# Optimization experiments

Hardware: AMD Instinct MI355X
Metric: run time of the kernel (lower is better)

## Reference

```python
import jax, jax.numpy as jnp
import numpy as np
from jax import lax

B, L, P, CIN, N, HD, PH, K = 2048, 96, 96, 8, 64, 64, 8, 3
DIM_C = CIN * N  # 512


def _silu(x):
    return x * jax.nn.sigmoid(x)


def _lin(x, w, b):
    return x @ w.T + b


def setup_inputs() -> dict:
    key = jax.random.key(0)
    ks = iter(jax.random.split(key, 64))

    def w(shape):
        fan_in = shape[-1]
        return (jax.random.normal(next(ks), shape, jnp.float32) / np.sqrt(fan_in)).astype(jnp.float32)

    inp = {"x": jax.random.normal(next(ks), (B, L, CIN), jnp.float32)}
    # x_proj: 5 Linears (enc_in->h, h->h, h->h, h->h, h->N), SiLU between (dropout=eval/identity)
    inp["xp_w0"] = w((HD, CIN)); inp["xp_b0"] = jnp.zeros((HD,), jnp.float32)
    inp["xp_w1"] = w((HD, HD));  inp["xp_b1"] = jnp.zeros((HD,), jnp.float32)
    inp["xp_w2"] = w((HD, HD));  inp["xp_b2"] = jnp.zeros((HD,), jnp.float32)
    inp["xp_w3"] = w((HD, HD));  inp["xp_b3"] = jnp.zeros((HD,), jnp.float32)
    inp["xp_w4"] = w((N, HD));   inp["xp_b4"] = jnp.zeros((N,), jnp.float32)
    # x_proj_: Linear(N,h), SiLU, Linear(h,N)
    inp["xpp_w0"] = w((HD, N)); inp["xpp_b0"] = jnp.zeros((HD,), jnp.float32)
    inp["xpp_w1"] = w((N, HD)); inp["xpp_b1"] = jnp.zeros((N,), jnp.float32)
    # depthwise dilated Conv1d: weight (N, 1, K)
    inp["conv_w"] = w((N, 1, K)); inp["conv_b"] = jnp.zeros((N,), jnp.float32)
    inp["span_A"] = jnp.asarray(0.1, jnp.float32)
    # compress: Linear(N*L, PH)
    inp["comp_w"] = w((PH, N * L)); inp["comp_b"] = jnp.zeros((PH,), jnp.float32)
    # a_ode.net: Linear(PH,h), SiLU, Linear(h,PH), Tanh
    inp["net_w0"] = w((HD, PH)); inp["net_b0"] = jnp.zeros((HD,), jnp.float32)
    inp["net_w1"] = w((PH, HD)); inp["net_b1"] = jnp.zeros((PH,), jnp.float32)
    # lat2out: Linear(PH,8), SiLU, Linear(8,N)
    inp["lo_w0"] = w((8, PH)); inp["lo_b0"] = jnp.zeros((8,), jnp.float32)
    inp["lo_w1"] = w((N, 8));  inp["lo_b1"] = jnp.zeros((N,), jnp.float32)
    # lat2out_c: Linear(PH,8), SiLU, Linear(8, CIN*N)
    inp["lc_w0"] = w((8, PH));     inp["lc_b0"] = jnp.zeros((8,), jnp.float32)
    inp["lc_w1"] = w((DIM_C, 8));  inp["lc_b1"] = jnp.zeros((DIM_C,), jnp.float32)
    # lat2out_z: Linear(N,N), SiLU, Linear(N, CIN)
    inp["lz_w0"] = w((N, N));   inp["lz_b0"] = jnp.zeros((N,), jnp.float32)
    inp["lz_w1"] = w((CIN, N)); inp["lz_b1"] = jnp.zeros((CIN,), jnp.float32)
    return inp


def reference(x, xp_w0, xp_b0, xp_w1, xp_b1, xp_w2, xp_b2, xp_w3, xp_b3, xp_w4, xp_b4,
              xpp_w0, xpp_b0, xpp_w1, xpp_b1, conv_w, conv_b, span_A, comp_w, comp_b,
              net_w0, net_b0, net_w1, net_b1, lo_w0, lo_b0, lo_w1, lo_b1,
              lc_w0, lc_b0, lc_w1, lc_b1, lz_w0, lz_b0, lz_w1, lz_b1):
    Bsz = x.shape[0]

    def x_proj(t):
        h = _silu(_lin(t, xp_w0, xp_b0))
        h = _silu(_lin(h, xp_w1, xp_b1))
        h = _silu(_lin(h, xp_w2, xp_b2))
        h = _silu(_lin(h, xp_w3, xp_b3))
        return _lin(h, xp_w4, xp_b4)

    x_old = x_proj(x[:, :L])                       # (B, L, N)
    hist = x_old.transpose(0, 2, 1)                # (B, N, L)
    pad = (K - 1) * 2                              # 4
    conv = lax.conv_general_dilated(
        hist, conv_w, window_strides=(1,), padding=[(pad, pad)],
        rhs_dilation=(2,), dimension_numbers=("NCH", "OIH", "NCH"),
        feature_group_count=N) + conv_b[None, :, None]
    hist = _silu(conv)[:, :, -L:]                  # (B, N, L)
    hist_f = hist.transpose(0, 2, 1).reshape(Bsz, L * N)
    vector_F = _lin(hist_f, comp_w, comp_b)        # (B, PH)

    a0 = vector_F
    z0 = x_proj(x[:, L - 1])                       # (B, N)

    # Householder matrix H = I - 2 v v^T with v = normalize(x_proj_(z0))
    v = _lin(_silu(_lin(z0, xpp_w0, xpp_b0)), xpp_w1, xpp_b1)
    v = v / (jnp.linalg.norm(v, axis=-1, keepdims=True) + 1e-8)
    Hh = jnp.eye(N, dtype=x.dtype)[None] - 2.0 * v[:, :, None] * v[:, None, :]  # (B,N,N)

    dt = jnp.clip(span_A, 1e-8, 7.0)               # uniform Euler step size
    s0 = jnp.concatenate([a0, z0], axis=-1)        # (B, PH+N)

    def step(s, _):
        a = s[:, :PH]
        z = s[:, PH:]
        da = jnp.tanh(_lin(_silu(_lin(a, net_w0, net_b0)), net_w1, net_b1))  # (B,PH)
        d = _lin(_silu(_lin(a, lo_w0, lo_b0)), lo_w1, lo_b1)                 # (B,N)
        # dz = H^T diag(d) H z   (fused; avoids materializing A_mat)
        Hz = jnp.einsum('bjk,bk->bj', Hh, z)
        dz = jnp.einsum('bj,bji->bi', d * Hz, Hh)
        s_new = s + dt * jnp.concatenate([da, dz], axis=-1)
        return s_new, s_new

    _, sol = lax.scan(step, s0, None, length=P)    # (P, B, PH+N) == sol[1:]

    c_traj = sol[:, :, :PH]                        # (P, B, PH)
    z_traj = sol[:, :, PH:]                        # (P, B, N)

    C = _lin(_silu(_lin(c_traj, lc_w0, lc_b0)), lc_w1, lc_b1)  # (P, B, CIN*N)
    C = C.reshape(P, Bsz, CIN, N)
    y_hat_c = jnp.einsum('pbcn,pbn->pbc', C, z_traj)           # (P, B, CIN)
    added_z = _lin(_silu(_lin(z_traj, lz_w0, lz_b0)), lz_w1, lz_b1)
    x_pred = (y_hat_c + added_z).transpose(1, 0, 2)            # (B, P, CIN)

    x_rec = x[:, :L, :]
    return (x_rec, x_pred)
```

## Files before the change

### kernel.cpp

```cpp
#include <hip/hip_runtime.h>
#include <cstdint>
#include <cstddef>

#define BB 2048
#define LL 96
#define PP 96
#define NN 64
#define HSTRIDE 68

typedef __attribute__((ext_vector_type(8))) short short8;
typedef __attribute__((ext_vector_type(4))) float f32x4;

union U4S8 { uint4 u; short8 s; };

__device__ __forceinline__ float siluf(float x) {
  return x * __builtin_amdgcn_rcpf(1.0f + __expf(-x));
}
__device__ __forceinline__ float tanhf_fast(float x) {
  return 1.0f - 2.0f * __builtin_amdgcn_rcpf(1.0f + __expf(2.0f * x));
}
__device__ __forceinline__ float rlane(float x, int l) {
  return __int_as_float(__builtin_amdgcn_readlane(__float_as_int(x), l));
}

template <int CTRL>
__device__ __forceinline__ float dppadd(float x) {
  int y = __builtin_amdgcn_update_dpp(0, __float_as_int(x), CTRL, 0xF, 0xF, false);
  return x + __int_as_float(y);
}
template <int CTRL>
__device__ __forceinline__ float dppmov(float x) {
  int y = __builtin_amdgcn_update_dpp(0, __float_as_int(x), CTRL, 0xF, 0xF, false);
  return __int_as_float(y);
}

__device__ __forceinline__ float addswap16(float x) {
#if __has_builtin(__builtin_amdgcn_permlane16_swap)
  auto r = __builtin_amdgcn_permlane16_swap(__float_as_uint(x), __float_as_uint(x), false, false);
  return __uint_as_float(r[0]) + __uint_as_float(r[1]);
#else
  return x + __shfl_xor(x, 16, 64);
#endif
}
__device__ __forceinline__ float addswap32(float x) {
#if __has_builtin(__builtin_amdgcn_permlane32_swap)
  auto r = __builtin_amdgcn_permlane32_swap(__float_as_uint(x), __float_as_uint(x), false, false);
  return __uint_as_float(r[0]) + __uint_as_float(r[1]);
#else
  return x + __shfl_xor(x, 32, 64);
#endif
}
__device__ __forceinline__ float movswap32(float x, bool hi) {
#if __has_builtin(__builtin_amdgcn_permlane32_swap)
  auto r = __builtin_amdgcn_permlane32_swap(__float_as_uint(x), __float_as_uint(x), false, false);
  return __uint_as_float(hi ? r[0] : r[1]);
#else
  return __shfl_xor(x, 32, 64);
#endif
}

__device__ __forceinline__ float wave_sum(float x) {
  x = dppadd<0xB1>(x);
  x = dppadd<0x4E>(x);
  x = dppadd<0x141>(x);
  x = dppadd<0x128>(x);
  x = addswap16(x);
  x = addswap32(x);
  return x;
}

__device__ __forceinline__ uint32_t packsplit(float f) {
  uint32_t b = __float_as_uint(f);
  uint32_t h = b & 0xFFFF0000u;
  float r = f - __uint_as_float(h);
  return h | (__float_as_uint(r) >> 16);
}
__device__ __forceinline__ void splitpack2(float f0, float f1, uint32_t& dhi, uint32_t& dlo) {
  uint32_t b0 = __float_as_uint(f0), b1 = __float_as_uint(f1);
  uint32_t h0 = b0 & 0xFFFF0000u, h1 = b1 & 0xFFFF0000u;
  float r0 = f0 - __uint_as_float(h0), r1 = f1 - __uint_as_float(h1);
  dhi = (h0 >> 16) | h1;
  dlo = (__float_as_uint(r0) >> 16) | (__float_as_uint(r1) & 0xFFFF0000u);
}
__device__ __forceinline__ void unpack2(uint32_t p0, uint32_t p1, uint32_t& dhi, uint32_t& dlo) {
  dhi = (p0 >> 16) | (p1 & 0xFFFF0000u);
  dlo = (p0 & 0xFFFFu) | (p1 << 16);
}
__device__ __forceinline__ void readfrag(const uint32_t* p, short8& hi, short8& lo) {
  uint4 pa = *(const uint4*)p;
  uint4 pb = *(const uint4*)(p + 4);
  U4S8 h, l;
  unpack2(pa.x, pa.y, h.u.x, l.u.x);
  unpack2(pa.z, pa.w, h.u.y, l.u.y);
  unpack2(pb.x, pb.y, h.u.z, l.u.z);
  unpack2(pb.z, pb.w, h.u.w, l.u.w);
  hi = h.s; lo = l.s;
}
__device__ __forceinline__ f32x4 mm_split(f32x4 acc, const short8* Ah, const short8* Al,
                                          const short8* Bh, const short8* Bl) {
  acc = __builtin_amdgcn_mfma_f32_16x16x32_bf16(Ah[0], Bh[0], acc, 0, 0, 0);
  acc = __builtin_amdgcn_mfma_f32_16x16x32_bf16(Ah[1], Bh[1], acc, 0, 0, 0);
  acc = __builtin_amdgcn_mfma_f32_16x16x32_bf16(Al[0], Bh[0], acc, 0, 0, 0);
  acc = __builtin_amdgcn_mfma_f32_16x16x32_bf16(Al[1], Bh[1], acc, 0, 0, 0);
  acc = __builtin_amdgcn_mfma_f32_16x16x32_bf16(Ah[0], Bl[0], acc, 0, 0, 0);
  acc = __builtin_amdgcn_mfma_f32_16x16x32_bf16(Ah[1], Bl[1], acc, 0, 0, 0);
  return acc;
}

__global__ __launch_bounds__(256, 2) void k_xproj(
    const float* __restrict__ x,
    const float* __restrict__ w0, const float* __restrict__ b0,
    const float* __restrict__ w1, const float* __restrict__ b1,
    const float* __restrict__ w2, const float* __restrict__ b2,
    const float* __restrict__ w3, const float* __restrict__ b3,
    const float* __restrict__ w4, const float* __restrict__ b4,
    float* __restrict__ x_old, float* __restrict__ out)
{
  __shared__ uint32_t hbuf[128 * HSTRIDE];
  __shared__ uint32_t wbufA[64 * HSTRIDE];
  __shared__ uint32_t wbufB[64 * HSTRIDE];
  __shared__ float bs[320];

  int tid = threadIdx.x;
  int wave = tid >> 6, lane = tid & 63;
  int quad = lane >> 4, m16 = lane & 15;
  size_t tokBase = (size_t)blockIdx.x * 128;

  {
    size_t e = tokBase * 8 + (size_t)tid * 4;
    *(float4*)(out + e) = *(const float4*)(x + e);
  }
  if (tid < 64) {
    bs[tid]       = b0[tid];
    bs[64 + tid]  = b1[tid];
    bs[128 + tid] = b2[tid];
    bs[192 + tid] = b3[tid];
    bs[256 + tid] = b4[tid];
  }
  #pragma unroll
  for (int i = 0; i < 4; ++i) {
    int e4 = i * 256 + tid;
    int o = e4 >> 4, k = (e4 & 15) << 2;
    float4 wv = ((const float4*)w1)[e4];
    *(uint4*)(wbufA + o * HSTRIDE + k) =
        make_uint4(packsplit(wv.x), packsplit(wv.y), packsplit(wv.z), packsplit(wv.w));
  }
  __syncthreads();

  short8 A0h[2], A0l[2];
  #pragma unroll
  for (int mt = 0; mt < 2; ++mt) {
    U4S8 h, l;
    h.u = make_uint4(0, 0, 0, 0); l.u = make_uint4(0, 0, 0, 0);
    if (quad == 0) {
      const float* xp = x + (tokBase + wave * 32 + mt * 16 + m16) * 8;
      float4 xa = *(const float4*)xp;
      float4 xb = *(const float4*)(xp + 4);
      splitpack2(xa.x, xa.y, h.u.x, l.u.x);
      splitpack2(xa.z, xa.w, h.u.y, l.u.y);
      splitpack2(xb.x, xb.y, h.u.z, l.u.z);
      splitpack2(xb.z, xb.w, h.u.w, l.u.w);
    }
    A0h[mt] = h.s; A0l[mt] = l.s;
  }
  short8 B0h[4], B0l[4];
  #pragma unroll
  for (int nt = 0; nt < 4; ++nt) {
    U4S8 h, l;
    h.u = make_uint4(0, 0, 0, 0); l.u = make_uint4(0, 0, 0, 0);
    if (quad == 0) {
      const float* wp = w0 + (nt * 16 + m16) * 8;
      float4 wa = *(const float4*)wp;
      float4 wb = *(const float4*)(wp + 4);
      splitpack2(wa.x, wa.y, h.u.x, l.u.x);
      splitpack2(wa.z, wa.w, h.u.y, l.u.y);
      splitpack2(wb.x, wb.y, h.u.z, l.u.z);
      splitpack2(wb.z, wb.w, h.u.w, l.u.w);
    }
    B0h[nt] = h.s; B0l[nt] = l.s;
  }
  {
    f32x4 acc[2][4];
    #pragma unroll
    for (int mt = 0; mt < 2; ++mt)
      #pragma unroll
      for (int nt = 0; nt < 4; ++nt) {
        float bv = bs[nt * 16 + m16];
        acc[mt][nt] = (f32x4){bv, bv, bv, bv};
      }
    #pragma unroll
    for (int mt = 0; mt < 2; ++mt)
      #pragma unroll
      for (int nt = 0; nt < 4; ++nt)
        acc[mt][nt] = __builtin_amdgcn_mfma_f32_16x16x32_bf16(A0h[mt], B0h[nt], acc[mt][nt], 0, 0, 0);
    #pragma unroll
    for (int mt = 0; mt < 2; ++mt)
      #pragma unroll
      for (int nt = 0; nt < 4; ++nt)
        acc[mt][nt] = __builtin_amdgcn_mfma_f32_16x16x32_bf16(A0l[mt], B0h[nt], acc[mt][nt], 0, 0, 0);
    #pragma unroll
    for (int mt = 0; mt < 2; ++mt)
      #pragma unroll
      for (int nt = 0; nt < 4; ++nt)
        acc[mt][nt] = __builtin_amdgcn_mfma_f32_16x16x32_bf16(A0h[mt], B0l[nt], acc[mt][nt], 0, 0, 0);
    #pragma unroll
    for (int mt = 0; mt < 2; ++mt)
      #pragma unroll
      for (int nt = 0; nt < 4; ++nt)
        #pragma unroll
        for (int r = 0; r < 4; ++r) {
          float s = siluf(acc[mt][nt][r]);
          hbuf[(wave * 32 + mt * 16 + quad * 4 + r) * HSTRIDE + nt * 16 + m16] = packsplit(s);
        }
  }

  const float* Ws[4] = {w1, w2, w3, w4};
  uint32_t* cur = wbufA;
  uint32_t* nxt = wbufB;
  #pragma unroll 1
  for (int lyr = 0; lyr < 4; ++lyr) {
    float4 wv[4];
    if (lyr < 3) {
      const float* wn = Ws[lyr + 1];
      #pragma unroll
      for (int i = 0; i < 4; ++i) wv[i] = ((const float4*)wn)[i * 256 + tid];
    }
    short8 Bh[8], Bl[8];
    #pragma unroll
    for (int nt = 0; nt < 4; ++nt)
      #pragma unroll
      for (int ks = 0; ks < 2; ++ks)
        readfrag(cur + (nt * 16 + m16) * HSTRIDE + ks * 32 + quad * 8, Bh[nt * 2 + ks], Bl[nt * 2 + ks]);
    short8 Ah[4], Al[4];
    #pragma unroll
    for (int mt = 0; mt < 2; ++mt)
      #pragma unroll
      for (int ks = 0; ks < 2; ++ks)
        readfrag(hbuf + (wave * 32 + mt * 16 + m16) * HSTRIDE + ks * 32 + quad * 8, Ah[mt * 2 + ks], Al[mt * 2 + ks]);

    f32x4 acc[2][4];
    #pragma unroll
    for (int mt = 0; mt < 2; ++mt)
      #pragma unroll
      for (int nt = 0; nt < 4; ++nt) {
        float bv = bs[(lyr + 1) * 64 + nt * 16 + m16];
        acc[mt][nt] = (f32x4){bv, bv, bv, bv};
      }
    #pragma unroll
    for (int ks = 0; ks < 2; ++ks)
      #pragma unroll
      for (int mt = 0; mt < 2; ++mt)
        #pragma unroll
        for (int nt = 0; nt < 4; ++nt)
          acc[mt][nt] = __builtin_amdgcn_mfma_f32_16x16x32_bf16(Ah[mt * 2 + ks], Bh[nt * 2 + ks], acc[mt][nt], 0, 0, 0);
    #pragma unroll
    for (int ks = 0; ks < 2; ++ks)
      #pragma unroll
      for (int mt = 0; mt < 2; ++mt)
        #pragma unroll
        for (int nt = 0; nt < 4; ++nt)
          acc[mt][nt] = __builtin_amdgcn_mfma_f32_16x16x32_bf16(Al[mt * 2 + ks], Bh[nt * 2 + ks], acc[mt][nt], 0, 0, 0);
    #pragma unroll
    for (int ks = 0; ks < 2; ++ks)
      #pragma unroll
      for (int mt = 0; mt < 2; ++mt)
        #pragma unroll
        for (int nt = 0; nt < 4; ++nt)
          acc[mt][nt] = __builtin_amdgcn_mfma_f32_16x16x32_bf16(Ah[mt * 2 + ks], Bl[nt * 2 + ks], acc[mt][nt], 0, 0, 0);

    if (lyr < 3) {
      #pragma unroll
      for (int i = 0; i < 4; ++i) {
        int e4 = i * 256 + tid;
        int o = e4 >> 4, k = (e4 & 15) << 2;
        *(uint4*)(nxt + o * HSTRIDE + k) =
            make_uint4(packsplit(wv[i].x), packsplit(wv[i].y), packsplit(wv[i].z), packsplit(wv[i].w));
      }
    }

    if (lyr < 3) {
      #pragma unroll
      for (int mt = 0; mt < 2; ++mt)
        #pragma unroll
        for (int nt = 0; nt < 4; ++nt)
          #pragma unroll
          for (int r = 0; r < 4; ++r) {
            float s = siluf(acc[mt][nt][r]);
            hbuf[(wave * 32 + mt * 16 + quad * 4 + r) * HSTRIDE + nt * 16 + m16] = packsplit(s);
          }
    } else {
      #pragma unroll
      for (int mt = 0; mt < 2; ++mt)
        #pragma unroll
        for (int nt = 0; nt < 4; ++nt)
          #pragma unroll
          for (int r = 0; r < 4; ++r) {
            size_t t = tokBase + wave * 32 + mt * 16 + quad * 4 + r;
            x_old[t * 64 + nt * 16 + m16] = acc[mt][nt][r];
          }
    }
    __syncthreads();
    uint32_t* tmp = cur; cur = nxt; nxt = tmp;
  }
}

__global__ __launch_bounds__(256) void k_hist(
    const float* __restrict__ x_old,
    const float* __restrict__ conv_w, const float* __restrict__ conv_b,
    const float* __restrict__ comp_w, const float* __restrict__ comp_b,
    const float* __restrict__ xw0, const float* __restrict__ xb0,
    const float* __restrict__ xw1, const float* __restrict__ xb1,
    float* __restrict__ a0_o, float* __restrict__ v_o, float* __restrict__ z0_o)
{
  __shared__ float xo[LL * NN];
  __shared__ float red[32];
  __shared__ float hbuf[64];
  int b = blockIdx.x, tid = threadIdx.x;
  const float* src = x_old + (size_t)b * (LL * NN);
  #pragma unroll
  for (int i = 0; i < 6; ++i) {
    int e = (i * 256 + tid) * 4;
    *(float4*)(xo + e) = *(const float4*)(src + e);
  }
  __syncthreads();
  int c = tid & 63;
  float cw0 = conv_w[c * 3], cw1 = conv_w[c * 3 + 1], cw2 = conv_w[c * 3 + 2];
  float cb = conv_b[c];
  float acc[8];
  #pragma unroll
  for (int q = 0; q < 8; ++q) acc[q] = 0.f;
  #pragma unroll 1
  for (int j = 0; j < 24; ++j) {
    int e = j * 256 + tid;
    int t = e >> 6;
    float s = xo[t * 64 + c] * cw0 + cb;
    if (t + 2 < LL) s += xo[(t + 2) * 64 + c] * cw1;
    if (t + 4 < LL) s += xo[(t + 4) * 64 + c] * cw2;
    float hv = siluf(s);
    #pragma unroll
    for (int q = 0; q < 8; ++q) acc[q] += hv * comp_w[q * 6144 + e];
  }
  #pragma unroll
  for (int q = 0; q < 8; ++q) acc[q] = dppadd<0xB1>(acc[q]);
  #pragma unroll
  for (int q = 0; q < 8; ++q) acc[q] = dppadd<0x4E>(acc[q]);
  #pragma unroll
  for (int q = 0; q < 8; ++q) acc[q] = dppadd<0x141>(acc[q]);
  #pragma unroll
  for (int q = 0; q < 8; ++q) acc[q] = dppadd<0x128>(acc[q]);
  #pragma unroll
  for (int q = 0; q < 8; ++q) acc[q] = addswap16(acc[q]);
  #pragma unroll
  for (int q = 0; q < 8; ++q) acc[q] = addswap32(acc[q]);
  int wave = tid >> 6, lane = tid & 63;
  if (lane < 8) {
    float sel = acc[0];
    #pragma unroll
    for (int q = 1; q < 8; ++q) sel = (lane == q) ? acc[q] : sel;
    red[wave * 8 + lane] = sel;
  }
  __syncthreads();
  if (tid < 8)
    a0_o[b * 8 + tid] = red[tid] + red[8 + tid] + red[16 + tid] + red[24 + tid] + comp_b[tid];
  if (tid < 64) {
    float a2 = xb0[tid];
    #pragma unroll 8
    for (int k = 0; k < 64; ++k) a2 += xw0[tid * 64 + k] * xo[6080 + k];
    hbuf[tid] = siluf(a2);
  }
  __syncthreads();
  float vr = 0.f;
  if (tid < 64) {
    vr = xb1[tid];
    #pragma unroll 8
    for (int k = 0; k < 64; ++k) vr += xw1[tid * 64 + k] * hbuf[k];
  }
  float s2 = wave_sum(vr * vr);
  if (tid < 64) {
    float nrm = sqrtf(s2) + 1e-8f;
    v_o[b * 64 + tid] = vr / nrm;
    z0_o[b * 64 + tid] = xo[6080 + tid];
  }
}

__global__ __launch_bounds__(256) void k_scan(
    const float* __restrict__ a0_i, const float* __restrict__ v_i, const float* __restrict__ z0_i,
    const float* __restrict__ nw0, const float* __restrict__ nb0_p,
    const float* __restrict__ nw1, const float* __restrict__ nb1_p,
    const float* __restrict__ lw0, const float* __restrict__ lb0_p,
    const float* __restrict__ lw1, const float* __restrict__ lb1_p,
    const float* __restrict__ spanA, float* __restrict__ atraj, uint32_t* __restrict__ ztraj)
{
  int tid = threadIdx.x;
  int lane = tid & 63;
  int wv = tid >> 6;
  int b = blockIdx.x * 4 + wv;
  float dt = fminf(fmaxf(spanA[0], 1e-8f), 7.0f);
  int i8 = lane & 7;
  bool hi32 = lane >= 32;
  int rrow = ((lane ^ (lane >> 1)) & 1) | (((lane ^ (lane >> 2)) & 1) << 1) | (((lane >> 5) & 1) << 2);

  float w0r[8], wxl[4], wxp[4], g0r[8], d1r[8];
  #pragma unroll
  for (int i = 0; i < 8; ++i) w0r[i] = nw0[lane * 8 + i];
  #pragma unroll
  for (int j = 0; j < 4; ++j) wxl[j] = nw1[rrow * 64 + (lane ^ j)];
  #pragma unroll
  for (int j = 0; j < 4; ++j) wxp[j] = nw1[(rrow ^ 4) * 64 + (lane ^ j)];
  #pragma unroll
  for (int i = 0; i < 8; ++i) g0r[i] = lw0[i8 * 8 + i];
  #pragma unroll
  for (int i = 0; i < 8; ++i) d1r[i] = lw1[lane * 8 + i];
  float nb0 = nb0_p[lane];
  float nb1r = nb1_p[rrow];
  float lb0o = lb0_p[i8];
  float lb1 = lb1_p[lane];
  float v = v_i[b * 64 + lane];
  float z = z0_i[b * 64 + lane];
  float a_own = a0_i[b * 8 + rrow];
  float t0 = wave_sum(v * z);
  float w = z - 2.0f * t0 * v;
  float a_s[8];
  a_s[0] = rlane(a_own, 0);  a_s[1] = rlane(a_own, 2);
  a_s[2] = rlane(a_own, 4);  a_s[3] = rlane(a_own, 6);
  a_s[4] = rlane(a_own, 32); a_s[5] = rlane(a_own, 34);
  a_s[6] = rlane(a_own, 36); a_s[7] = rlane(a_own, 38);

  float* ab = atraj + (size_t)b * (PP * 8);
  uint32_t* zb = ztraj + (size_t)b * (PP * NN);
  bool astore = (lane & 0x19) == 0;

  auto step_rec = [&]() {
    float u0 = w0r[0] * a_s[0] + w0r[1] * a_s[1];
    float u1 = w0r[2] * a_s[2] + w0r[3] * a_s[3];
    float u2 = w0r[4] * a_s[4] + w0r[5] * a_s[5];
    float u3 = w0r[6] * a_s[6] + w0r[7] * a_s[7];
    float h = siluf(nb0 + ((u0 + u1) + (u2 + u3)));
    float hv1 = dppmov<0xB1>(h);
    float hv2 = dppmov<0x4E>(h);
    float hv3 = dppmov<0x1B>(h);
    float slo = (wxl[0] * h + wxl[1] * hv1) + (wxl[2] * hv2 + wxl[3] * hv3);
    float pre = (wxp[0] * h + wxp[1] * hv1) + (wxp[2] * hv2 + wxp[3] * hv3);
    float ps = slo + movswap32(pre, hi32);
    ps = dppadd<0x141>(ps);
    ps = dppadd<0x128>(ps);
    ps = addswap16(ps);
    float da = tanhf_fast(ps + nb1r);
    float e0 = g0r[0] * a_s[0] + g0r[1] * a_s[1];
    float e1 = g0r[2] * a_s[2] + g0r[3] * a_s[3];
    float e2 = g0r[4] * a_s[4] + g0r[5] * a_s[5];
    float e3 = g0r[6] * a_s[6] + g0r[7] * a_s[7];
    float g_own = siluf(lb0o + ((e0 + e1) + (e2 + e3)));
    float f0 = d1r[0] * rlane(g_own, 0) + d1r[1] * rlane(g_own, 1);
    float f1 = d1r[2] * rlane(g_own, 2) + d1r[3] * rlane(g_own, 3);
    float f2 = d1r[4] * rlane(g_own, 4) + d1r[5] * rlane(g_own, 5);
    float f3 = d1r[6] * rlane(g_own, 6) + d1r[7] * rlane(g_own, 7);
    float d = lb1 + ((f0 + f1) + (f2 + f3));
    a_own += dt * da;
    a_s[0] = rlane(a_own, 0);  a_s[1] = rlane(a_own, 2);
    a_s[2] = rlane(a_own, 4);  a_s[3] = rlane(a_own, 6);
    a_s[4] = rlane(a_own, 32); a_s[5] = rlane(a_own, 34);
    a_s[6] = rlane(a_own, 36); a_s[7] = rlane(a_own, 38);
    w *= (1.0f + dt * d);
  };

  step_rec();
  float wo = w, ao = a_own;
  #pragma unroll 1
  for (int p = 1; p < PP; ++p) {
    float woc = wo, aoc = ao;
    step_rec();
    wo = w; ao = a_own;
    float t1 = wave_sum(v * woc);
    float zv = woc - 2.0f * t1 * v;
    if (astore) ab[(p - 1) * 8 + rrow] = aoc;
    zb[(p - 1) * 64 + lane] = packsplit(zv);
  }
  {
    float t1 = wave_sum(v * wo);
    float zv = wo - 2.0f * t1 * v;
    if (astore) ab[(PP - 1) * 8 + rrow] = ao;
    zb[(PP - 1) * 64 + lane] = packsplit(zv);
  }
}

__global__ __launch_bounds__(256, 4) void k_post(
    const float* __restrict__ atraj, const uint32_t* __restrict__ ztraj,
    const float* __restrict__ cw0, const float* __restrict__ cb0,
    const float* __restrict__ cw1, const float* __restrict__ cb1,
    const float* __restrict__ zw0, const float* __restrict__ zb0,
    const float* __restrict__ zw1, const float* __restrict__ zb1,
    float* __restrict__ out)
{
  __shared__ uint32_t wbuf[144 * HSTRIDE];
  __shared__ float    cw0s[64];
  __shared__ float    cb0s[8];
  __shared__ float    zb0s[64];
  __shared__ float    zb1s[8];

  int tid = threadIdx.x;
  int wave = tid >> 6, lane = tid & 63;
  int quad = lane >> 4, m16 = lane & 15;
  size_t tokBase = (size_t)blockIdx.x * 64;

  #pragma unroll
  for (int i = 0; i < 36; ++i) {
    int e = i * 256 + tid;
    int o = e >> 6, k = e & 63;
    float wv;
    if (o < 64)       wv = cw1[(((o >> 3) * 64 + k) << 3) + (o & 7)];
    else if (o < 72)  wv = cb1[(o - 64) * 64 + k];
    else if (o < 136) wv = zw0[(o - 72) * 64 + k];
    else              wv = zw1[(o - 136) * 64 + k];
    wbuf[o * HSTRIDE + k] = packsplit(wv);
  }
  if (tid < 64) cw0s[tid] = cw0[tid];
  if (tid < 8)  cb0s[tid] = cb0[tid];
  if (tid < 64) zb0s[tid] = zb0[tid];
  if (tid < 8)  zb1s[tid] = zb1[tid];
  __syncthreads();

  const uint32_t* zp = ztraj + (tokBase + wave * 16 + m16) * 64;
  short8 Ah[2], Al[2];
  readfrag(zp + quad * 8,      Ah[0], Al[0]);
  readfrag(zp + 32 + quad * 8, Ah[1], Al[1]);

  f32x4 acc1[5];
  #pragma unroll
  for (int nt = 0; nt < 5; ++nt) {
    short8 Bh[2], Bl[2];
    readfrag(wbuf + (nt * 16 + m16) * HSTRIDE + quad * 8,      Bh[0], Bl[0]);
    readfrag(wbuf + (nt * 16 + m16) * HSTRIDE + 32 + quad * 8, Bh[1], Bl[1]);
    f32x4 acc = (f32x4){0.f, 0.f, 0.f, 0.f};
    acc1[nt] = mm_split(acc, Ah, Al, Bh, Bl);
  }
  __syncthreads();

  uint32_t* ebuf = wbuf;
  #pragma unroll
  for (int nt = 0; nt < 4; ++nt) {
    short8 Bh[2], Bl[2];
    readfrag(wbuf + (72 + nt * 16 + m16) * HSTRIDE + quad * 8,      Bh[0], Bl[0]);
    readfrag(wbuf + (72 + nt * 16 + m16) * HSTRIDE + 32 + quad * 8, Bh[1], Bl[1]);
    f32x4 acc = (f32x4){0.f, 0.f, 0.f, 0.f};
    acc = mm_split(acc, Ah, Al, Bh, Bl);
    int m = nt * 16 + m16;
    float zbv = zb0s[m];
    #pragma unroll
    for (int r = 0; r < 4; ++r) {
      float e = siluf(acc[r] + zbv);
      ebuf[(wave * 16 + quad * 4 + r) * HSTRIDE + m] = packsplit(e);
    }
  }

  f32x4 acc3;
  {
    short8 Eh[2], El[2];
    readfrag(ebuf + (wave * 16 + m16) * HSTRIDE + quad * 8,      Eh[0], El[0]);
    readfrag(ebuf + (wave * 16 + m16) * HSTRIDE + 32 + quad * 8, Eh[1], El[1]);
    short8 Bh[2], Bl[2];
    int brow = 136 + (m16 & 7);
    readfrag(wbuf + brow * HSTRIDE + quad * 8,      Bh[0], Bl[0]);
    readfrag(wbuf + brow * HSTRIDE + 32 + quad * 8, Bh[1], Bl[1]);
    f32x4 acc = (f32x4){0.f, 0.f, 0.f, 0.f};
    acc3 = mm_split(acc, Eh, El, Bh, Bl);
  }

  int j = m16 & 7;
  float cwj[8];
  #pragma unroll
  for (int i = 0; i < 8; ++i) cwj[i] = cw0s[j * 8 + i];
  float cbj = cb0s[j];
  #pragma unroll
  for (int r = 0; r < 4; ++r) {
    size_t idx = tokBase + wave * 16 + quad * 4 + r;
    const float* ap = atraj + idx * 8;
    float4 a0v = *(const float4*)ap;
    float4 a1v = *(const float4*)(ap + 4);
    float g2v = cbj
      + cwj[0] * a0v.x + cwj[1] * a0v.y + cwj[2] * a0v.z + cwj[3] * a0v.w
      + cwj[4] * a1v.x + cwj[5] * a1v.y + cwj[6] * a1v.z + cwj[7] * a1v.w;
    g2v = siluf(g2v);
    float yc[4], qo[4];
    #pragma unroll
    for (int nt = 0; nt < 4; ++nt) {
      float p = acc1[nt][r] * g2v;
      p = dppadd<0xB1>(p);
      p = dppadd<0x4E>(p);
      p = dppadd<0x141>(p);
      yc[nt] = p;
      qo[nt] = dppmov<0x128>(p);
    }
    if (m16 < 8) {
      int cc = m16;
      int nt = cc >> 1;
      float ye = (nt == 0) ? yc[0] : (nt == 1) ? yc[1] : (nt == 2) ? yc[2] : yc[3];
      float yo = (nt == 0) ? qo[0] : (nt == 1) ? qo[1] : (nt == 2) ? qo[2] : qo[3];
      float y = (cc & 1) ? yo : ye;
      y += acc1[4][r] + acc3[r] + zb1s[cc];
      out[(size_t)(BB * LL * 8) + idx * 8 + cc] = y;
    }
  }
}

extern "C" void kernel_launch(void* const* d_in, const int* in_sizes, int n_in,
                              void* d_out, int out_size, void* d_ws, size_t ws_size,
                              hipStream_t stream) {
  const float* x      = (const float*)d_in[0];
  const float* xp_w0  = (const float*)d_in[1];
  const float* xp_b0  = (const float*)d_in[2];
  const float* xp_w1  = (const float*)d_in[3];
  const float* xp_b1  = (const float*)d_in[4];
  const float* xp_w2  = (const float*)d_in[5];
  const float* xp_b2  = (const float*)d_in[6];
  const float* xp_w3  = (const float*)d_in[7];
  const float* xp_b3  = (const float*)d_in[8];
  const float* xp_w4  = (const float*)d_in[9];
  const float* xp_b4  = (const float*)d_in[10];
  const float* xpp_w0 = (const float*)d_in[11];
  const float* xpp_b0 = (const float*)d_in[12];
  const float* xpp_w1 = (const float*)d_in[13];
  const float* xpp_b1 = (const float*)d_in[14];
  const float* conv_w = (const float*)d_in[15];
  const float* conv_b = (const float*)d_in[16];
  const float* span_A = (const float*)d_in[17];
  const float* comp_w = (const float*)d_in[18];
  const float* comp_b = (const float*)d_in[19];
  const float* net_w0 = (const float*)d_in[20];
  const float* net_b0 = (const float*)d_in[21];
  const float* net_w1 = (const float*)d_in[22];
  const float* net_b1 = (const float*)d_in[23];
  const float* lo_w0  = (const float*)d_in[24];
  const float* lo_b0  = (const float*)d_in[25];
  const float* lo_w1  = (const float*)d_in[26];
  const float* lo_b1  = (const float*)d_in[27];
  const float* lc_w0  = (const float*)d_in[28];
  const float* lc_b0  = (const float*)d_in[29];
  const float* lc_w1  = (const float*)d_in[30];
  const float* lc_b1  = (const float*)d_in[31];
  const float* lz_w0  = (const float*)d_in[32];
  const float* lz_b0  = (const float*)d_in[33];
  const float* lz_w1  = (const float*)d_in[34];
  const float* lz_b1  = (const float*)d_in[35];

  float*    ws    = (float*)d_ws;
  float*    x_old = ws;
  uint32_t* ztraj = (uint32_t*)ws;
  float*    atraj = ws + 12582912;
  float*    a0    = ws + 14155776;
  float*    vv    = a0 + 2048 * 8;
  float*    z0    = vv + 2048 * 64;
  float*    out   = (float*)d_out;

  hipLaunchKernelGGL(k_xproj, dim3(1536), dim3(256), 0, stream,
                     x, xp_w0, xp_b0, xp_w1, xp_b1, xp_w2, xp_b2, xp_w3, xp_b3,
                     xp_w4, xp_b4, x_old, out);
  hipLaunchKernelGGL(k_hist, dim3(2048), dim3(256), 0, stream,
                     x_old, conv_w, conv_b, comp_w, comp_b,
                     xpp_w0, xpp_b0, xpp_w1, xpp_b1, a0, vv, z0);
  hipLaunchKernelGGL(k_scan, dim3(512), dim3(256), 0, stream,
                     a0, vv, z0, net_w0, net_b0, net_w1, net_b1,
                     lo_w0, lo_b0, lo_w1, lo_b1, span_A, atraj, ztraj);
  hipLaunchKernelGGL(k_post, dim3(3072), dim3(256), 0, stream,
                     atraj, ztraj, lc_w0, lc_b0, lc_w1, lc_b1,
                     lz_w0, lz_b0, lz_w1, lz_b1, out);
}
```

Baseline: 303.7 us.

## Interleave hi/lo bf16 pairs along K to fold split-precision MFMA passes

Values are stored as interleaved (hi,lo) bf16 pairs along the K dimension instead of separate hi and lo fragments. One MFMA with paired A and B then computes Ah*Bh+Al*Bl, and a second MFMA with 16-bit-rotated A adds Al*Bh+Ah*Bl. This replaces the three-pass split-bf16 scheme and removes the unpack shuffles in readfrag. The cost is twice the K length per MFMA and an extra lo*lo term, which changes the numerics slightly and doubles fragment register use in the MLP layers.

```diff
diff --git a/kernel.cpp b/kernel.cpp
--- a/kernel.cpp
+++ b/kernel.cpp
@@ -75,6 +75,24 @@
   float r = f - __uint_as_float(h);
   return h | (__float_as_uint(r) >> 16);
 }
+__device__ __forceinline__ uint32_t packpair(float f) {
+  uint32_t b = __float_as_uint(f);
+  uint32_t h = b & 0xFFFF0000u;
+  float r = f - __uint_as_float(h);
+  return (h >> 16) | (__float_as_uint(r) & 0xFFFF0000u);
+}
+__device__ __forceinline__ uint32_t rot16(uint32_t x) {
+#if __has_builtin(__builtin_amdgcn_alignbit)
+  return __builtin_amdgcn_alignbit(x, x, 16);
+#else
+  return (x >> 16) | (x << 16);
+#endif
+}
+__device__ __forceinline__ uint4 rot16x4(uint4 u) {
+  return make_uint4(rot16(u.x), rot16(u.y), rot16(u.z), rot16(u.w));
+}
+__device__ __forceinline__ short8 as8(uint4 u) { U4S8 c; c.u = u; return c.s; }
+
 __device__ __forceinline__ void splitpack2(float f0, float f1, uint32_t& dhi, uint32_t& dlo) {
   uint32_t b0 = __float_as_uint(f0), b1 = __float_as_uint(f1);
   uint32_t h0 = b0 & 0xFFFF0000u, h1 = b1 & 0xFFFF0000u;
@@ -143,41 +161,31 @@
     int o = e4 >> 4, k = (e4 & 15) << 2;
     float4 wv = ((const float4*)w1)[e4];
     *(uint4*)(wbufA + o * HSTRIDE + k) =
-        make_uint4(packsplit(wv.x), packsplit(wv.y), packsplit(wv.z), packsplit(wv.w));
+        make_uint4(packpair(wv.x), packpair(wv.y), packpair(wv.z), packpair(wv.w));
   }
   __syncthreads();
 
-  short8 A0h[2], A0l[2];
+  uint4 A0[2];
   #pragma unroll
   for (int mt = 0; mt < 2; ++mt) {
-    U4S8 h, l;
-    h.u = make_uint4(0, 0, 0, 0); l.u = make_uint4(0, 0, 0, 0);
-    if (quad == 0) {
-      const float* xp = x + (tokBase + wave * 32 + mt * 16 + m16) * 8;
+    uint4 t = make_uint4(0, 0, 0, 0);
+    if (quad < 2) {
+      const float* xp = x + (tokBase + wave * 32 + mt * 16 + m16) * 8 + quad * 4;
       float4 xa = *(const float4*)xp;
-      float4 xb = *(const float4*)(xp + 4);
-      splitpack2(xa.x, xa.y, h.u.x, l.u.x);
-      splitpack2(xa.z, xa.w, h.u.y, l.u.y);
-      splitpack2(xb.x, xb.y, h.u.z, l.u.z);
-      splitpack2(xb.z, xb.w, h.u.w, l.u.w);
-    }
-    A0h[mt] = h.s; A0l[mt] = l.s;
-  }
-  short8 B0h[4], B0l[4];
+      t = make_uint4(packpair(xa.x), packpair(xa.y), packpair(xa.z), packpair(xa.w));
+    }
+    A0[mt] = t;
+  }
+  uint4 B0[4];
   #pragma unroll
   for (int nt = 0; nt < 4; ++nt) {
-    U4S8 h, l;
-    h.u = make_uint4(0, 0, 0, 0); l.u = make_uint4(0, 0, 0, 0);
-    if (quad == 0) {
-      const float* wp = w0 + (nt * 16 + m16) * 8;
+    uint4 t = make_uint4(0, 0, 0, 0);
+    if (quad < 2) {
+      const float* wp = w0 + (nt * 16 + m16) * 8 + quad * 4;
       float4 wa = *(const float4*)wp;
-      float4 wb = *(const float4*)(wp + 4);
-      splitpack2(wa.x, wa.y, h.u.x, l.u.x);
-      splitpack2(wa.z, wa.w, h.u.y, l.u.y);
-      splitpack2(wb.x, wb.y, h.u.z, l.u.z);
-      splitpack2(wb.z, wb.w, h.u.w, l.u.w);
-    }
-    B0h[nt] = h.s; B0l[nt] = l.s;
+      t = make_uint4(packpair(wa.x), packpair(wa.y), packpair(wa.z), packpair(wa.w));
+    }
+    B0[nt] = t;
   }
   {
     f32x4 acc[2][4];
@@ -192,17 +200,14 @@
     for (int mt = 0; mt < 2; ++mt)
       #pragma unroll
       for (int nt = 0; nt < 4; ++nt)
-        acc[mt][nt] = __builtin_amdgcn_mfma_f32_16x16x32_bf16(A0h[mt], B0h[nt], acc[mt][nt], 0, 0, 0);
-    #pragma unroll
-    for (int mt = 0; mt < 2; ++mt)
+        acc[mt][nt] = __builtin_amdgcn_mfma_f32_16x16x32_bf16(as8(A0[mt]), as8(B0[nt]), acc[mt][nt], 0, 0, 0);
+    #pragma unroll
+    for (int mt = 0; mt < 2; ++mt) {
+      uint4 As = rot16x4(A0[mt]);
       #pragma unroll
       for (int nt = 0; nt < 4; ++nt)
-        acc[mt][nt] = __builtin_amdgcn_mfma_f32_16x16x32_bf16(A0l[mt], B0h[nt], acc[mt][nt], 0, 0, 0);
-    #pragma unroll
-    for (int mt = 0; mt < 2; ++mt)
-      #pragma unroll
-      for (int nt = 0; nt < 4; ++nt)
-        acc[mt][nt] = __builtin_amdgcn_mfma_f32_16x16x32_bf16(A0h[mt], B0l[nt], acc[mt][nt], 0, 0, 0);
+        acc[mt][nt] = __builtin_amdgcn_mfma_f32_16x16x32_bf16(as8(As), as8(B0[nt]), acc[mt][nt], 0, 0, 0);
+    }
     #pragma unroll
     for (int mt = 0; mt < 2; ++mt)
       #pragma unroll
@@ -210,7 +215,7 @@
         #pragma unroll
         for (int r = 0; r < 4; ++r) {
           float s = siluf(acc[mt][nt][r]);
-          hbuf[(wave * 32 + mt * 16 + quad * 4 + r) * HSTRIDE + nt * 16 + m16] = packsplit(s);
+          hbuf[(wave * 32 + mt * 16 + quad * 4 + r) * HSTRIDE + nt * 16 + m16] = packpair(s);
         }
   }
 
@@ -225,18 +230,18 @@
       #pragma unroll
       for (int i = 0; i < 4; ++i) wv[i] = ((const float4*)wn)[i * 256 + tid];
     }
-    short8 Bh[8], Bl[8];
+    uint4 Bf[16];
     #pragma unroll
     for (int nt = 0; nt < 4; ++nt)
       #pragma unroll
-      for (int ks = 0; ks < 2; ++ks)
-        readfrag(cur + (nt * 16 + m16) * HSTRIDE + ks * 32 + quad * 8, Bh[nt * 2 + ks], Bl[nt * 2 + ks]);
-    short8 Ah[4], Al[4];
+      for (int c = 0; c < 4; ++c)
+        Bf[nt * 4 + c] = *(const uint4*)(cur + (nt * 16 + m16) * HSTRIDE + c * 16 + quad * 4);
+    uint4 Af[8];
     #pragma unroll
     for (int mt = 0; mt < 2; ++mt)
       #pragma unroll
-      for (int ks = 0; ks < 2; ++ks)
-        readfrag(hbuf + (wave * 32 + mt * 16 + m16) * HSTRIDE + ks * 32 + quad * 8, Ah[mt * 2 + ks], Al[mt * 2 + ks]);
+      for (int c = 0; c < 4; ++c)
+        Af[mt * 4 + c] = *(const uint4*)(hbuf + (wave * 32 + mt * 16 + m16) * HSTRIDE + c * 16 + quad * 4);
 
     f32x4 acc[2][4];
     #pragma unroll
@@ -247,26 +252,21 @@
         acc[mt][nt] = (f32x4){bv, bv, bv, bv};
       }
     #pragma unroll
-    for (int ks = 0; ks < 2; ++ks)
+    for (int c = 0; c < 4; ++c)
       #pragma unroll
       for (int mt = 0; mt < 2; ++mt)
         #pragma unroll
         for (int nt = 0; nt < 4; ++nt)
-          acc[mt][nt] = __builtin_amdgcn_mfma_f32_16x16x32_bf16(Ah[mt * 2 + ks], Bh[nt * 2 + ks], acc[mt][nt], 0, 0, 0);
-    #pragma unroll
-    for (int ks = 0; ks < 2; ++ks)
-      #pragma unroll
-      for (int mt = 0; mt < 2; ++mt)
+          acc[mt][nt] = __builtin_amdgcn_mfma_f32_16x16x32_bf16(as8(Af[mt * 4 + c]), as8(Bf[nt * 4 + c]), acc[mt][nt], 0, 0, 0);
+    #pragma unroll
+    for (int c = 0; c < 4; ++c)
+      #pragma unroll
+      for (int mt = 0; mt < 2; ++mt) {
+        uint4 As = rot16x4(Af[mt * 4 + c]);
         #pragma unroll
         for (int nt = 0; nt < 4; ++nt)
-          acc[mt][nt] = __builtin_amdgcn_mfma_f32_16x16x32_bf16(Al[mt * 2 + ks], Bh[nt * 2 + ks], acc[mt][nt], 0, 0, 0);
-    #pragma unroll
-    for (int ks = 0; ks < 2; ++ks)
-      #pragma unroll
-      for (int mt = 0; mt < 2; ++mt)
-        #pragma unroll
-        for (int nt = 0; nt < 4; ++nt)
-          acc[mt][nt] = __builtin_amdgcn_mfma_f32_16x16x32_bf16(Ah[mt * 2 + ks], Bl[nt * 2 + ks], acc[mt][nt], 0, 0, 0);
+          acc[mt][nt] = __builtin_amdgcn_mfma_f32_16x16x32_bf16(as8(As), as8(Bf[nt * 4 + c]), acc[mt][nt], 0, 0, 0);
+      }
 
     if (lyr < 3) {
       #pragma unroll
@@ -274,7 +274,7 @@
         int e4 = i * 256 + tid;
         int o = e4 >> 4, k = (e4 & 15) << 2;
         *(uint4*)(nxt + o * HSTRIDE + k) =
-            make_uint4(packsplit(wv[i].x), packsplit(wv[i].y), packsplit(wv[i].z), packsplit(wv[i].w));
+            make_uint4(packpair(wv[i].x), packpair(wv[i].y), packpair(wv[i].z), packpair(wv[i].w));
       }
     }
 
@@ -286,7 +286,7 @@
           #pragma unroll
           for (int r = 0; r < 4; ++r) {
             float s = siluf(acc[mt][nt][r]);
-            hbuf[(wave * 32 + mt * 16 + quad * 4 + r) * HSTRIDE + nt * 16 + m16] = packsplit(s);
+            hbuf[(wave * 32 + mt * 16 + quad * 4 + r) * HSTRIDE + nt * 16 + m16] = packpair(s);
           }
     } else {
       #pragma unroll
```

New measurement: 297.4 us. 1.02x faster.
